# Kernel optimization log

Measured on AMD Instinct MI355X. Metric: run time of the kernel, lower is better.

Reference implementation:

```python
import jax, jax.numpy as jnp
import numpy as np

B, N, K = 4, 20480, 16
LAMDA = 2.0  # config.lfa_param

def _gather(pc, idx):
    # pc: [B, N, D], idx: [B, N, K] -> [B, N, K, D]
    return jax.vmap(lambda p, i: p[i])(pc, idx)

def _cbr(x, W, g, b, act=True):
    # 1x1 conv (no bias) + BN(eval, affine) + optional ReLU; x: [B, C, N, K]
    y = jnp.einsum('oc,bcnk->bonk', W, x)
    y = y * g[None, :, None, None] + b[None, :, None, None]
    return jnp.maximum(y, 0.0) if act else y

def _fdis(feat, f_nb):
    # feat: [B, C, N], f_nb: [B, C, N, K] -> exp(-mean_c |diff|): [B, 1, N, K]
    return jnp.exp(-jnp.mean(jnp.abs(feat[..., None] - f_nb), axis=1, keepdims=True))

def _pool(f_set, f_dis, g_dis, fcW, mW, mg, mb):
    # Dualdis_Att_Pool: softmax attention over neighbor dim K
    concat = jnp.concatenate([g_dis, f_dis * LAMDA, f_set], axis=1)
    att = jax.nn.softmax(jnp.einsum('oc,bcnk->bonk', fcW, concat), axis=3)
    f_lc = jnp.sum(f_set * att, axis=-1, keepdims=True)
    return _cbr(f_lc, mW, mg, mb)

def _forward(feature, xyz, m1_W, m1_g, m1_b, lm1_W, lm1_g, lm1_b, lm2_W, lm2_g, lm2_b, p1fc_W, p1m_W, p1m_g, p1m_b, p2fc_W, p2m_W, p2m_g, p2m_b, m2_W, m2_g, m2_b, sc_W, sc_g, sc_b, m3_W, m3_g, m3_b, m4_W, m4_g, m4_b, neigh_idx):
    f_pc = _cbr(feature, m1_W, m1_g, m1_b)               # [B,16,N,1]
    # --- local polar representation ---
    nb = _gather(xyz, neigh_idx)                         # [B,N,K,3]
    xyz_t = xyz[:, :, None, :]
    rel = xyz_t - nb
    r_alpha = jnp.arctan2(rel[..., 1], rel[..., 0])[..., None]
    r_beta = jnp.arctan2(rel[..., 2], jnp.sqrt(rel[..., 0]**2 + rel[..., 1]**2))[..., None]
    r_dis = jnp.sqrt(jnp.sum(rel * rel, axis=-1, keepdims=True))
    rel_info = jnp.concatenate([r_dis, jnp.broadcast_to(xyz_t, nb.shape), nb], axis=-1)
    g_dis = jnp.exp(-r_dis)                              # [B,N,K,1]
    local_vol = jnp.max(r_dis[..., 0], axis=-1) ** 3     # [B,N]
    dirv = xyz - jnp.mean(nb, axis=2)                    # [B,N,3]
    d_alpha = jnp.arctan2(dirv[..., 1], dirv[..., 0])[:, :, None, None]
    d_beta = jnp.arctan2(dirv[..., 2], jnp.sqrt(dirv[..., 0]**2 + dirv[..., 1]**2))[:, :, None, None]
    angle = jnp.concatenate([r_alpha - d_alpha, r_beta - d_beta], axis=-1)
    local_rep = jnp.concatenate([angle, rel_info], axis=-1)  # [B,N,K,9]
    g_vol = jnp.sqrt(jnp.sum(xyz * xyz, axis=-1)) ** 3
    lg_ratio = (local_vol / g_vol)[..., None]            # [B,N,1]
    g_dis = jnp.transpose(g_dis, (0, 3, 1, 2))           # [B,1,N,K]
    lrep = _cbr(jnp.transpose(local_rep, (0, 3, 1, 2)), lm1_W, lm1_g, lm1_b)  # [B,16,N,K]
    # --- dual-distance attentive pooling 1 ---
    feat0 = f_pc[..., 0]
    f_nb = jnp.transpose(_gather(jnp.transpose(feat0, (0, 2, 1)), neigh_idx), (0, 3, 1, 2))
    f_cat = jnp.concatenate([f_nb, lrep], axis=1)        # [B,32,N,K]
    f_lc = _pool(f_cat, _fdis(feat0, f_nb), g_dis, p1fc_W, p1m_W, p1m_g, p1m_b)  # [B,16,N,1]
    # --- dual-distance attentive pooling 2 ---
    lrep2 = _cbr(lrep, lm2_W, lm2_g, lm2_b)
    feat1 = f_lc[..., 0]
    f_nb2 = jnp.transpose(_gather(jnp.transpose(feat1, (0, 2, 1)), neigh_idx), (0, 3, 1, 2))
    f_cat2 = jnp.concatenate([f_nb2, lrep2], axis=1)     # [B,32,N,K]
    f_lc2 = _pool(f_cat2, _fdis(feat1, f_nb2), g_dis, p2fc_W, p2m_W, p2m_g, p2m_b)  # [B,32,N,1]
    # --- residual head ---
    out_lc = _cbr(f_lc2, m2_W, m2_g, m2_b, act=False)
    sc = _cbr(feature, sc_W, sc_g, sc_b, act=False)
    f_gc_in = jnp.transpose(jnp.concatenate([xyz, lg_ratio], axis=-1), (0, 2, 1))[..., None]
    f_gc = _cbr(f_gc_in, m3_W, m3_g, m3_b, act=False)
    return _cbr(jnp.concatenate([out_lc + sc, f_gc], axis=1), m4_W, m4_g, m4_b)  # [B,64,N,1]

def setup_inputs():
    key = jax.random.key(0)
    ks = iter(jax.random.split(key, 48))
    def rn(shape, s=1.0):
        return jax.random.normal(next(ks), shape, jnp.float32) * s
    inp = {"feature": rn((B, 16, N, 1)), "xyz": rn((B, N, 3))}
    def wgb(name, co, ci):
        inp[name + "_W"] = rn((co, ci), 0.1)
        inp[name + "_g"] = jax.random.uniform(next(ks), (co,), jnp.float32, 0.5, 1.5)
        inp[name + "_b"] = jnp.zeros((co,), jnp.float32)
    wgb("m1", 16, 16); wgb("lm1", 16, 9); wgb("lm2", 16, 16)
    inp["p1fc_W"] = rn((32, 34), 0.1); wgb("p1m", 16, 32)
    inp["p2fc_W"] = rn((32, 34), 0.1); wgb("p2m", 32, 32)
    wgb("m2", 64, 32); wgb("sc", 64, 16); wgb("m3", 64, 4); wgb("m4", 64, 128)
    inp["neigh_idx"] = jax.random.randint(next(ks), (B, N, K), 0, N)
    return inp

def reference(feature, xyz, m1_W, m1_g, m1_b, lm1_W, lm1_g, lm1_b, lm2_W, lm2_g, lm2_b, p1fc_W, p1m_W, p1m_g, p1m_b, p2fc_W, p2m_W, p2m_g, p2m_b, m2_W, m2_g, m2_b, sc_W, sc_g, sc_b, m3_W, m3_g, m3_b, m4_W, m4_g, m4_b, neigh_idx):
    return _forward(feature, xyz, m1_W, m1_g, m1_b, lm1_W, lm1_g, lm1_b, lm2_W, lm2_g, lm2_b, p1fc_W, p1m_W, p1m_g, p1m_b, p2fc_W, p2m_W, p2m_g, p2m_b, m2_W, m2_g, m2_b, sc_W, sc_g, sc_b, m3_W, m3_g, m3_b, m4_W, m4_g, m4_b, neigh_idx)
```

## Files before the change

### kernel.cpp

```cpp
#include <hip/hip_runtime.h>

#define NN 20480
#define NPTS 81920
#define MS 36
#define RSH 40
#define PTSH 640
#define MIDOFF 2560
#define LOG2E 1.4426950408889634f

#define MIDO 0
#define ACTO 2304
#define HO   4608
#define LGRO 13056
#define SMTOT 13120

#define P1MWT 0
#define P2MWT 512
#define M2WT  1536
#define SCWT  3584
#define M3WT  4608
#define M4WT  4864
#define BFB   13056
#define WTOT  15104

typedef _Float16 half8 __attribute__((ext_vector_type(8)));
typedef float f32x4 __attribute__((ext_vector_type(4)));

__device__ __forceinline__ float redsum16(float v){
    v += __shfl_xor(v, 1); v += __shfl_xor(v, 2);
    v += __shfl_xor(v, 4); v += __shfl_xor(v, 8);
    return v;
}
__device__ __forceinline__ float redmax16(float v){
    v = fmaxf(v, __shfl_xor(v, 1)); v = fmaxf(v, __shfl_xor(v, 2));
    v = fmaxf(v, __shfl_xor(v, 4)); v = fmaxf(v, __shfl_xor(v, 8));
    return v;
}
__device__ __forceinline__ void wsync(){
    __builtin_amdgcn_wave_barrier();
    __threadfence_block();
    __builtin_amdgcn_wave_barrier();
}
__device__ __forceinline__ float frcp(float x){ return __builtin_amdgcn_rcpf(x); }

__device__ __forceinline__ unsigned int ph(float lo, float hi){
    union { _Float16 h[2]; unsigned int u; } cv;
    cv.h[0] = (_Float16)lo; cv.h[1] = (_Float16)hi;
    return cv.u;
}
__device__ __forceinline__ float2 unph(unsigned int u){
    union { unsigned int u; _Float16 h[2]; } cv; cv.u = u;
    return make_float2((float)cv.h[0], (float)cv.h[1]);
}
__device__ __forceinline__ float h2f(short s){
    union { short s; _Float16 h; } cv; cv.s = s;
    return (float)cv.h;
}

__device__ __forceinline__ float fatan2(float y, float x){
    float ax = fabsf(x), ay = fabsf(y);
    float mx = fmaxf(ax, ay), mn = fminf(ax, ay);
    float z = mn * frcp(mx);
    z = (mx == 0.f) ? 0.f : z;
    float z2 = z * z;
    float a = fmaf(0.05265332f, z2, -0.11643287f);
    a = fmaf(a, z2, 0.19354346f);
    a = fmaf(a, z2, -0.33262347f);
    a = fmaf(a, z2, 0.99997726f);
    a = a * z;
    a = (ay > ax) ? (1.5707963268f - a) : a;
    a = (x < 0.f) ? (3.1415926536f - a) : a;
    return (y < 0.f) ? -a : a;
}

__device__ __forceinline__ int swiz(int bid){
    int x = bid & 7, s = bid >> 3;
    return ((x >> 1) * 2560) + ((x & 1) * 1280) + s;
}
__device__ __forceinline__ int swizC(int bid){
    int x = bid & 7, s = bid >> 3;
    return x * 160 + s;
}

__global__ void k_fill4(float4* out, float val, int n4){
    int i = blockIdx.x * blockDim.x + threadIdx.x;
    int stride = gridDim.x * blockDim.x;
    float4 v = make_float4(val, val, val, val);
    for (; i < n4; i += stride) out[i] = v;
}

__global__ void k_prep(
    const float* __restrict__ p1fc, const float* __restrict__ p2fc,
    const float* __restrict__ p1mW, const float* __restrict__ p2mW,
    const float* __restrict__ m2W,  const float* __restrict__ scW,
    const float* __restrict__ m3W,  const float* __restrict__ m4W,
    float* __restrict__ wb)
{
    int bid = blockIdx.x;
    if (bid == 0){
        for (int e = threadIdx.x; e < 512; e += 256)
            wb[P1MWT + e] = p1mW[e];
    } else if (bid == 1){
        for (int e = threadIdx.x; e < 1024; e += 256){
            int c = e >> 5, r = e & 31;
            int k = r >> 1, h = r & 1;
            wb[P2MWT + e] = p2mW[(k + 16*h)*32 + c];
        }
    } else if (bid == 2){
        for (int e = threadIdx.x; e < 2048; e += 256){
            int c = e >> 6, r = e & 63;
            int k = r >> 2, j = r & 3;
            wb[M2WT + e] = m2W[(k + 16*j)*32 + c];
        }
    } else if (bid == 3){
        for (int e = threadIdx.x; e < 1024; e += 256){
            int c = e >> 6, r = e & 63;
            int k = r >> 2, j = r & 3;
            wb[SCWT + e] = scW[(k + 16*j)*16 + c];
        }
    } else if (bid == 4){
        for (int e = threadIdx.x; e < 256; e += 256){
            int c = e >> 6, r = e & 63;
            int k = r >> 2, j = r & 3;
            wb[M3WT + e] = m3W[(k + 16*j)*4 + c];
        }
    } else if (bid == 5){
        for (int e = threadIdx.x; e < 8192; e += 256){
            int c = e >> 6, r = e & 63;
            int k = r >> 2, j = r & 3;
            wb[M4WT + e] = m4W[(k + 16*j)*128 + c];
        }
    } else if (bid == 6 || bid == 7){
        const float* src = (bid == 6) ? p1fc : p2fc;
        short* dst = (short*)(wb + BFB) + (bid - 6) * 2048;
        for (int e = threadIdx.x; e < 2048; e += 256){
            int j = e & 7, l = (e >> 3) & 63, tq = (e >> 9) & 3;
            int q = tq & 1, t = tq >> 1;
            int kk = ((l >> 4) << 3) + j;
            int c = q*32 + kk;
            int o = (l & 15) + 16*t;
            float v = (c < 34) ? src[o*34 + c] * LOG2E : 0.f;
            union { _Float16 h; short s; } cv; cv.h = (_Float16)v;
            dst[e] = cv.s;
        }
    }
}

__global__ __launch_bounds__(256) void k_feat0(
    const float* __restrict__ featp,
    const float* __restrict__ m1W,
    const float* __restrict__ m1g,
    const float* __restrict__ m1b,
    float* __restrict__ feat0)
{
    int p = blockIdx.x * 256 + threadIdx.x;
    if (p >= NPTS) return;
    int b = p / NN;
    int n = p - b * NN;
    float x[16];
    #pragma unroll
    for (int c = 0; c < 16; c++) x[c] = featp[(b*16 + c)*NN + n];
    float* dst = feat0 + (size_t)p * 16;
    for (int o = 0; o < 16; o++){
        float acc = 0.f;
        #pragma unroll
        for (int c = 0; c < 16; c++) acc = fmaf(m1W[o*16 + c], x[c], acc);
        dst[o] = fmaxf(fmaf(m1g[o], acc, m1b[o]), 0.f);
    }
}

__device__ __forceinline__ float poolT(f32x4 a, const short* base, int c, int g){
    const short* xc = base + c;
    float x0 = h2f(xc[(g*4 + 0)*RSH]), x1 = h2f(xc[(g*4 + 1)*RSH]);
    float x2 = h2f(xc[(g*4 + 2)*RSH]), x3 = h2f(xc[(g*4 + 3)*RSH]);
    float m = fmaxf(fmaxf(a[0], a[1]), fmaxf(a[2], a[3]));
    m = fmaxf(m, __shfl_xor(m, 16)); m = fmaxf(m, __shfl_xor(m, 32));
    float e0 = exp2f(a[0] - m), e1 = exp2f(a[1] - m);
    float e2 = exp2f(a[2] - m), e3 = exp2f(a[3] - m);
    float s = (e0 + e1) + (e2 + e3);
    float num = fmaf(e3, x3, fmaf(e2, x2, fmaf(e1, x1, e0*x0)));
    s   += __shfl_xor(s, 16);   s   += __shfl_xor(s, 32);
    num += __shfl_xor(num, 16); num += __shfl_xor(num, 32);
    return num * frcp(s);
}

__device__ __forceinline__ void phaseB_mfma(
    const short* xs, const short* bfS, float* smMid, int tid)
{
    const half8* bf = (const half8*)bfS;
    const int l = tid & 63, wv = tid >> 6;
    const int o = l & 15, g = l >> 4;
    half8 B00 = bf[l], B01 = bf[64 + l], B10 = bf[128 + l], B11 = bf[192 + l];
    #pragma unroll 2
    for (int pp = 0; pp < 4; pp++){
        const int pt = wv*4 + pp;
        const short* base = xs + pt*PTSH;
        const short* rowp = base + (l & 15)*RSH;
        half8 A0 = *(const half8*)(rowp + g*8);
        unsigned int d = *(const unsigned int*)(rowp + 32);
        union { unsigned int u[4]; half8 v; } a1u;
        a1u.u[0] = (g == 0) ? d : 0u;
        a1u.u[1] = 0u; a1u.u[2] = 0u; a1u.u[3] = 0u;
        half8 A1 = a1u.v;
        f32x4 z = {0.f, 0.f, 0.f, 0.f};
        f32x4 a0 = __builtin_amdgcn_mfma_f32_16x16x32_f16(A0, B00, z, 0, 0, 0);
        a0       = __builtin_amdgcn_mfma_f32_16x16x32_f16(A1, B01, a0, 0, 0, 0);
        f32x4 a1 = __builtin_amdgcn_mfma_f32_16x16x32_f16(A0, B10, z, 0, 0, 0);
        a1       = __builtin_amdgcn_mfma_f32_16x16x32_f16(A1, B11, a1, 0, 0, 0);
        float mid0 = poolT(a0, base, 2 + o,      g);
        float mid1 = poolT(a1, base, 2 + o + 16, g);
        if (g == 0){
            smMid[pt*MS + o]      = mid0;
            smMid[pt*MS + o + 16] = mid1;
        }
    }
}

__global__ __launch_bounds__(128, 2) void k_stage1(
    const float* __restrict__ xyzp,
    const int* __restrict__ nidx,
    const float* __restrict__ feat0,
    const float* __restrict__ lm1W,
    const float* __restrict__ lm1g,
    const float* __restrict__ lm1b,
    const float* __restrict__ wb,
    const float* __restrict__ p1mg,
    const float* __restrict__ p1mb,
    float* __restrict__ feat1)
{
    __shared__ float sm[2848];
    short* xs = (short*)sm;
    const int k  = threadIdx.x & 15;
    const int pt = threadIdx.x >> 4;
    const int p  = (swiz(blockIdx.x) << 3) + pt;
    const int b  = p / NN;

    {
        const int ii = nidx[(p << 4) + k];
        const int q  = b * NN + ii;
        const float4* an = (const float4*)(feat0 + (size_t)q * 16);
        const float4* as = (const float4*)(feat0 + (size_t)p * 16);
        const float sx = xyzp[p*3 + 0];
        const float sy = xyzp[p*3 + 1];
        const float sz = xyzp[p*3 + 2];
        const float nx = xyzp[q*3 + 0];
        const float ny = xyzp[q*3 + 1];
        const float nz = xyzp[q*3 + 2];

        float4 A0 = an[0], A1 = an[1], A2 = an[2], A3 = an[3];
        float sd = 0.f;
        {
            float4 S0 = as[0], S1 = as[1], S2 = as[2], S3 = as[3];
            sd += fabsf(S0.x-A0.x) + fabsf(S0.y-A0.y) + fabsf(S0.z-A0.z) + fabsf(S0.w-A0.w);
            sd += fabsf(S1.x-A1.x) + fabsf(S1.y-A1.y) + fabsf(S1.z-A1.z) + fabsf(S1.w-A1.w);
            sd += fabsf(S2.x-A2.x) + fabsf(S2.y-A2.y) + fabsf(S2.z-A2.z) + fabsf(S2.w-A2.w);
            sd += fabsf(S3.x-A3.x) + fabsf(S3.y-A3.y) + fabsf(S3.z-A3.z) + fabsf(S3.w-A3.w);
        }
        float fdis2 = 2.f * __expf(-sd * 0.0625f);

        float rx = sx - nx, ry = sy - ny, rz = sz - nz;
        float r2 = rx*rx + ry*ry;
        float rdis = sqrtf(r2 + rz*rz);
        float ralpha = fatan2(ry, rx);
        float rbeta  = fatan2(rz, sqrtf(r2));
        float gdis = __expf(-rdis);

        float mx = redsum16(nx) * 0.0625f;
        float my = redsum16(ny) * 0.0625f;
        float mz = redsum16(nz) * 0.0625f;
        float dx = sx - mx, dy = sy - my, dz = sz - mz;
        float dalpha = fatan2(dy, dx);
        float dbeta  = fatan2(dz, sqrtf(dx*dx + dy*dy));

        float rep[9] = { ralpha - dalpha, rbeta - dbeta, rdis, sx, sy, sz, nx, ny, nz };
        float lrep[16];
        #pragma unroll
        for (int o = 0; o < 16; o++){
            float acc = 0.f;
            #pragma unroll
            for (int c = 0; c < 9; c++) acc = fmaf(lm1W[o*9 + c], rep[c], acc);
            lrep[o] = fmaxf(fmaf(lm1g[o], acc, lm1b[o]), 0.f);
        }

        uint4* rp = (uint4*)(xs + pt*PTSH + k*RSH);
        uint4 U;
        U.x = ph(gdis, fdis2); U.y = ph(A0.x, A0.y);
        U.z = ph(A0.z, A0.w);  U.w = ph(A1.x, A1.y);
        rp[0] = U;
        U.x = ph(A1.z, A1.w);  U.y = ph(A2.x, A2.y);
        U.z = ph(A2.z, A2.w);  U.w = ph(A3.x, A3.y);
        rp[1] = U;
        U.x = ph(A3.z, A3.w);      U.y = ph(lrep[0], lrep[1]);
        U.z = ph(lrep[2], lrep[3]); U.w = ph(lrep[4], lrep[5]);
        rp[2] = U;
        U.x = ph(lrep[6], lrep[7]);   U.y = ph(lrep[8], lrep[9]);
        U.z = ph(lrep[10], lrep[11]); U.w = ph(lrep[12], lrep[13]);
        rp[3] = U;
        U.x = ph(lrep[14], lrep[15]); U.y = 0u; U.z = 0u; U.w = 0u;
        rp[4] = U;
    }
    wsync();

    phaseB_mfma(xs, (const short*)(wb + BFB), sm + MIDOFF, threadIdx.x);
    wsync();

    {
        float mid[32];
        const float4* mp = (const float4*)(sm + MIDOFF + pt*MS);
        #pragma unroll
        for (int i = 0; i < 8; i++){
            float4 t = mp[i];
            mid[4*i]=t.x; mid[4*i+1]=t.y; mid[4*i+2]=t.z; mid[4*i+3]=t.w;
        }
        const float4* wp = (const float4*)(wb + P1MWT) + (k << 3);
        float acc = 0.f;
        #pragma unroll
        for (int i = 0; i < 8; i++){
            float4 wv = wp[i];
            acc = fmaf(wv.x, mid[4*i],   acc);
            acc = fmaf(wv.y, mid[4*i+1], acc);
            acc = fmaf(wv.z, mid[4*i+2], acc);
            acc = fmaf(wv.w, mid[4*i+3], acc);
        }
        feat1[(size_t)(p << 4) + k] = fmaxf(fmaf(p1mg[k], acc, p1mb[k]), 0.f);
    }
}

__global__ __launch_bounds__(128, 2) void k_s2ab(
    const float* __restrict__ xyzp,
    const int* __restrict__ nidx,
    const float* __restrict__ feat1,
    const float* __restrict__ lm1W,
    const float* __restrict__ lm1g,
    const float* __restrict__ lm1b,
    const float* __restrict__ lm2W,
    const float* __restrict__ lm2g,
    const float* __restrict__ lm2b,
    const float* __restrict__ wb,
    float* __restrict__ outp)
{
    __shared__ float sm[2848];
    short* xs = (short*)sm;
    const int k    = threadIdx.x & 15;
    const int pt   = threadIdx.x >> 4;
    const int pblk = swiz(blockIdx.x);
    const int p    = (pblk << 3) + pt;
    const int b    = p / NN;
    const int n    = p - b * NN;
    float lgrv;

    {
        const int ii = nidx[(p << 4) + k];
        const int q  = b * NN + ii;
        const float4* an = (const float4*)(feat1 + (size_t)q * 16);
        const float4* as = (const float4*)(feat1 + (size_t)p * 16);
        const float sx = xyzp[p*3 + 0];
        const float sy = xyzp[p*3 + 1];
        const float sz = xyzp[p*3 + 2];
        const float nx = xyzp[q*3 + 0];
        const float ny = xyzp[q*3 + 1];
        const float nz = xyzp[q*3 + 2];

        float4 A0 = an[0], A1 = an[1], A2 = an[2], A3 = an[3];
        float sd = 0.f;
        {
            float4 S0 = as[0], S1 = as[1], S2 = as[2], S3 = as[3];
            sd += fabsf(S0.x-A0.x) + fabsf(S0.y-A0.y) + fabsf(S0.z-A0.z) + fabsf(S0.w-A0.w);
            sd += fabsf(S1.x-A1.x) + fabsf(S1.y-A1.y) + fabsf(S1.z-A1.z) + fabsf(S1.w-A1.w);
            sd += fabsf(S2.x-A2.x) + fabsf(S2.y-A2.y) + fabsf(S2.z-A2.z) + fabsf(S2.w-A2.w);
            sd += fabsf(S3.x-A3.x) + fabsf(S3.y-A3.y) + fabsf(S3.z-A3.z) + fabsf(S3.w-A3.w);
        }
        float fdis2 = 2.f * __expf(-sd * 0.0625f);

        float rx = sx - nx, ry = sy - ny, rz = sz - nz;
        float r2 = rx*rx + ry*ry;
        float rdis = sqrtf(r2 + rz*rz);
        float ralpha = fatan2(ry, rx);
        float rbeta  = fatan2(rz, sqrtf(r2));
        float gdis = __expf(-rdis);

        float mx = redsum16(nx) * 0.0625f;
        float my = redsum16(ny) * 0.0625f;
        float mz = redsum16(nz) * 0.0625f;
        float dx = sx - mx, dy = sy - my, dz = sz - mz;
        float dalpha = fatan2(dy, dx);
        float dbeta  = fatan2(dz, sqrtf(dx*dx + dy*dy));

        float mxd = redmax16(rdis);
        float nr  = sqrtf(sx*sx + sy*sy + sz*sz);
        lgrv = (mxd*mxd*mxd) * frcp(nr*nr*nr);

        float rep[9] = { ralpha - dalpha, rbeta - dbeta, rdis, sx, sy, sz, nx, ny, nz };
        float lrep[16];
        #pragma unroll
        for (int o = 0; o < 16; o++){
            float acc = 0.f;
            #pragma unroll
            for (int c = 0; c < 9; c++) acc = fmaf(lm1W[o*9 + c], rep[c], acc);
            lrep[o] = fmaxf(fmaf(lm1g[o], acc, lm1b[o]), 0.f);
        }
        float lrep2[16];
        #pragma unroll
        for (int o = 0; o < 16; o++){
            float acc = 0.f;
            #pragma unroll
            for (int c = 0; c < 16; c++) acc = fmaf(lm2W[o*16 + c], lrep[c], acc);
            lrep2[o] = fmaxf(fmaf(lm2g[o], acc, lm2b[o]), 0.f);
        }

        uint4* rp = (uint4*)(xs + pt*PTSH + k*RSH);
        uint4 U;
        U.x = ph(gdis, fdis2); U.y = ph(A0.x, A0.y);
        U.z = ph(A0.z, A0.w);  U.w = ph(A1.x, A1.y);
        rp[0] = U;
        U.x = ph(A1.z, A1.w);  U.y = ph(A2.x, A2.y);
        U.z = ph(A2.z, A2.w);  U.w = ph(A3.x, A3.y);
        rp[1] = U;
        U.x = ph(A3.z, A3.w);        U.y = ph(lrep2[0], lrep2[1]);
        U.z = ph(lrep2[2], lrep2[3]); U.w = ph(lrep2[4], lrep2[5]);
        rp[2] = U;
        U.x = ph(lrep2[6], lrep2[7]);   U.y = ph(lrep2[8], lrep2[9]);
        U.z = ph(lrep2[10], lrep2[11]); U.w = ph(lrep2[12], lrep2[13]);
        rp[3] = U;
        U.x = ph(lrep2[14], lrep2[15]); U.y = 0u; U.z = 0u; U.w = 0u;
        rp[4] = U;
    }
    wsync();

    phaseB_mfma(xs, (const short*)(wb + BFB) + 2048, sm + MIDOFF, threadIdx.x);
    wsync();

    {
        float m0 = sm[MIDOFF + pt*MS + 2*k];
        float m1 = sm[MIDOFF + pt*MS + 2*k + 1];
        unsigned int u = ph(m0, m1);
        ((unsigned int*)outp)[(size_t)(b*64 + k)*NN + n] = u;
        if (k == 0) outp[(size_t)(b*64 + 16)*NN + n] = lgrv;
    }
}

__global__ __launch_bounds__(256, 2) void k_s2c(
    const float* __restrict__ featp,
    const float* __restrict__ xyzp,
    const float* __restrict__ wb,
    const float* __restrict__ p2mg,
    const float* __restrict__ p2mb,
    const float* __restrict__ m2g,
    const float* __restrict__ m2b,
    const float* __restrict__ scg,
    const float* __restrict__ scb,
    const float* __restrict__ m3g,
    const float* __restrict__ m3b,
    const float* __restrict__ m4g,
    const float* __restrict__ m4b,
    float* __restrict__ outp)
{
    __shared__ float sm[SMTOT];
    const int tid = threadIdx.x;
    const int k   = tid & 15;
    const int g   = (tid >> 4) & 3;
    const int w   = tid >> 6;
    const int pblk = swizC(blockIdx.x);
    const int p0  = pblk << 6;
    const int b   = p0 / NN;
    const int n0  = p0 - b * NN;
    const int ptw = w*16 + g*4;
    const int nT  = n0 + ptw;

    {
        uint4 um = *(const uint4*)((const unsigned int*)outp +
                                   (size_t)(b*64 + k)*NN + nT);
        float2 f;
        f = unph(um.x);
        sm[MIDO + (ptw+0)*36 + 2*k] = f.x; sm[MIDO + (ptw+0)*36 + 2*k+1] = f.y;
        f = unph(um.y);
        sm[MIDO + (ptw+1)*36 + 2*k] = f.x; sm[MIDO + (ptw+1)*36 + 2*k+1] = f.y;
        f = unph(um.z);
        sm[MIDO + (ptw+2)*36 + 2*k] = f.x; sm[MIDO + (ptw+2)*36 + 2*k+1] = f.y;
        f = unph(um.w);
        sm[MIDO + (ptw+3)*36 + 2*k] = f.x; sm[MIDO + (ptw+3)*36 + 2*k+1] = f.y;
        if (k == 0){
            float4 lv = *(const float4*)(outp + (size_t)(b*64 + 16)*NN + nT);
            sm[LGRO + ptw+0] = lv.x; sm[LGRO + ptw+1] = lv.y;
            sm[LGRO + ptw+2] = lv.z; sm[LGRO + ptw+3] = lv.w;
        }
    }
    wsync();

    {
        const float2* wp = (const float2*)(wb + P2MWT);
        float aA[4] = {0.f,0.f,0.f,0.f}, aB[4] = {0.f,0.f,0.f,0.f};
        #pragma unroll 2
        for (int cq = 0; cq < 8; cq++){
            f32x4 mv[4];
            #pragma unroll
            for (int i = 0; i < 4; i++)
                mv[i] = *(const f32x4*)(sm + MIDO + (ptw+i)*36 + cq*4);
            #pragma unroll
            for (int cc = 0; cc < 4; cc++){
                float2 wv = wp[(cq*4+cc)*16 + k];
                #pragma unroll
                for (int i = 0; i < 4; i++){
                    aA[i] = fmaf(wv.x, mv[i][cc], aA[i]);
                    aB[i] = fmaf(wv.y, mv[i][cc], aB[i]);
                }
            }
        }
        float gA = p2mg[k], bA = p2mb[k], gB = p2mg[k+16], bB = p2mb[k+16];
        #pragma unroll
        for (int i = 0; i < 4; i++){
            sm[ACTO + (ptw+i)*36 + k]      = fmaxf(fmaf(gA, aA[i], bA), 0.f);
            sm[ACTO + (ptw+i)*36 + k + 16] = fmaxf(fmaf(gB, aB[i], bB), 0.f);
        }
    }
    wsync();

    {
        const f32x4* w2 = (const f32x4*)(wb + M2WT);
        float hAc[4][4];
        #pragma unroll
        for (int j = 0; j < 4; j++)
            #pragma unroll
            for (int i = 0; i < 4; i++) hAc[j][i] = 0.f;
        #pragma unroll 2
        for (int cq = 0; cq < 8; cq++){
            f32x4 av[4];
            #pragma unroll
            for (int i = 0; i < 4; i++)
                av[i] = *(const f32x4*)(sm + ACTO + (ptw+i)*36 + cq*4);
            #pragma unroll
            for (int cc = 0; cc < 4; cc++){
                f32x4 wv = w2[(cq*4+cc)*16 + k];
                #pragma unroll
                for (int i = 0; i < 4; i++){
                    #pragma unroll
                    for (int j = 0; j < 4; j++)
                        hAc[j][i] = fmaf(wv[j], av[i][cc], hAc[j][i]);
                }
            }
        }
        const f32x4* ws = (const f32x4*)(wb + SCWT);
        float sAc[4][4];
        #pragma unroll
        for (int j = 0; j < 4; j++)
            #pragma unroll
            for (int i = 0; i < 4; i++) sAc[j][i] = 0.f;
        #pragma unroll 2
        for (int c = 0; c < 16; c++){
            f32x4 wv = ws[c*16 + k];
            f32x4 xv = *(const f32x4*)(featp + (size_t)(b*16 + c)*NN + nT);
            #pragma unroll
            for (int i = 0; i < 4; i++){
                #pragma unroll
                for (int j = 0; j < 4; j++)
                    sAc[j][i] = fmaf(wv[j], xv[i], sAc[j][i]);
            }
        }
        const f32x4* w3 = (const f32x4*)(wb + M3WT);
        float mAc[4][4];
        #pragma unroll
        for (int j = 0; j < 4; j++)
            #pragma unroll
            for (int i = 0; i < 4; i++) mAc[j][i] = 0.f;
        #pragma unroll
        for (int c = 0; c < 3; c++){
            f32x4 wv = w3[c*16 + k];
            #pragma unroll
            for (int i = 0; i < 4; i++){
                float vc = xyzp[(size_t)(p0 + ptw + i)*3 + c];
                #pragma unroll
                for (int j = 0; j < 4; j++)
                    mAc[j][i] = fmaf(wv[j], vc, mAc[j][i]);
            }
        }
        {
            f32x4 wv = w3[3*16 + k];
            #pragma unroll
            for (int i = 0; i < 4; i++){
                float vc = sm[LGRO + ptw + i];
                #pragma unroll
                for (int j = 0; j < 4; j++)
                    mAc[j][i] = fmaf(wv[j], vc, mAc[j][i]);
            }
        }
        #pragma unroll
        for (int j = 0; j < 4; j++){
            int oo = k + 16*j;
            float g2 = m2g[oo], b2 = m2b[oo];
            float gs = scg[oo], bs = scb[oo];
            float g3 = m3g[oo], b3 = m3b[oo];
            #pragma unroll
            for (int i = 0; i < 4; i++){
                float hv = fmaf(g2, hAc[j][i], b2) + fmaf(gs, sAc[j][i], bs);
                sm[HO + (ptw+i)*132 + oo]      = hv;
                sm[HO + (ptw+i)*132 + 64 + oo] = fmaf(g3, mAc[j][i], b3);
            }
        }
    }
    wsync();

    float acc[4][4];
    #pragma unroll
    for (int j = 0; j < 4; j++)
        #pragma unroll
        for (int i = 0; i < 4; i++) acc[j][i] = 0.f;
    {
        const f32x4* w4 = (const f32x4*)(wb + M4WT);
        #pragma unroll 4
        for (int cb = 0; cb < 32; cb++){
            f32x4 wj[4];
            #pragma unroll
            for (int cc = 0; cc < 4; cc++)
                wj[cc] = w4[(cb*4+cc)*16 + k];
            f32x4 hv[4];
            #pragma unroll
            for (int i = 0; i < 4; i++)
                hv[i] = *(const f32x4*)(sm + HO + (ptw+i)*132 + cb*4);
            #pragma unroll
            for (int cc = 0; cc < 4; cc++){
                #pragma unroll
                for (int i = 0; i < 4; i++){
                    #pragma unroll
                    for (int j = 0; j < 4; j++)
                        acc[j][i] = fmaf(wj[cc][j], hv[i][cc], acc[j][i]);
                }
            }
        }
    }
    {
        float* stg = sm + HO + w*16*132;
        #pragma unroll
        for (int j = 0; j < 4; j++){
            int oo = k + 16*j;
            float gv = m4g[oo], bv = m4b[oo];
            #pragma unroll
            for (int i = 0; i < 4; i++)
                stg[oo*20 + g*4 + i] = fmaxf(fmaf(gv, acc[j][i], bv), 0.f);
        }
        wsync();
        const int l = tid & 63;
        float* dst = outp + (size_t)(b*64 + l)*NN + n0 + w*16;
        #pragma unroll
        for (int q = 0; q < 4; q++){
            f32x4 v = *(const f32x4*)(stg + l*20 + q*4);
            *(f32x4*)(dst + q*4) = v;
        }
    }
}

extern "C" void kernel_launch(void* const* d_in, const int* in_sizes, int n_in,
                              void* d_out, int out_size, void* d_ws, size_t ws_size,
                              hipStream_t stream) {
    float* outp = (float*)d_out;

    float fillv = 1.0f;
    bool ok = true;
    if (n_in != 32) { fillv = 5.0f; ok = false; }
    else if (in_sizes[0] != 1310720 || in_sizes[1] != 245760 ||
             in_sizes[31] != 1310720) { fillv = 7.0f; ok = false; }
    else if (out_size != 5242880) { fillv = 9.0f; ok = false; }
    else if (ws_size < ((size_t)NPTS * 16 + WTOT) * sizeof(float)) { fillv = 11.0f; ok = false; }

    k_fill4<<<1024, 256, 0, stream>>>((float4*)outp, fillv, out_size/4);
    if (!ok) return;

    const float* featp = (const float*)d_in[0];
    const float* xyzp  = (const float*)d_in[1];
    const int*   nidx  = (const int*)d_in[31];

    float* feat0 = (float*)d_out;
    float* feat1 = (float*)d_ws;
    float* wb    = (float*)d_ws + (size_t)NPTS * 16;

    #define W(i) ((const float*)d_in[2 + (i)])
    k_prep<<<8, 256, 0, stream>>>(W(9), W(13), W(10), W(14), W(17), W(20),
                                  W(23), W(26), wb);
    k_feat0<<<NPTS/256, 256, 0, stream>>>(featp, W(0), W(1), W(2), feat0);
    k_stage1<<<NPTS/8, 128, 0, stream>>>(xyzp, nidx, feat0,
        W(3), W(4), W(5), wb, W(11), W(12), feat1);
    k_s2ab<<<NPTS/8, 128, 0, stream>>>(xyzp, nidx, feat1,
        W(3), W(4), W(5),
        W(6), W(7), W(8),
        wb, outp);
    k_s2c<<<NPTS/64, 256, 0, stream>>>(featp, xyzp, wb,
        W(15), W(16),
        W(18), W(19),
        W(21), W(22),
        W(24), W(25),
        W(27), W(28),
        outp);
    #undef W
}
```

Before: 265.9 us.

## Fold m2/sc/m3 linear layers into m4 weights and stage weights in LDS

Since m2, shortcut and m3 are linear with affine BN and no activation before m4, their weights are pre-multiplied into the m4 weights in k_prep, with a folded constant bias. k_s2c then computes the final 64 outputs directly from the activation, feature and xyz inputs, skipping the 128-wide intermediate and its matmul. Folded weights are copied into LDS per block. The output fill kernel now runs only on the error path, and k_feat0 writes with float4 stores. This changes float rounding order and adds a block-wide sync for the weight staging.

```diff
diff --git a/kernel.cpp b/kernel.cpp
--- a/kernel.cpp
+++ b/kernel.cpp
@@ -8,20 +8,24 @@
 #define MIDOFF 2560
 #define LOG2E 1.4426950408889634f
 
-#define MIDO 0
-#define ACTO 2304
-#define HO   4608
-#define LGRO 13056
-#define SMTOT 13120
-
 #define P1MWT 0
 #define P2MWT 512
-#define M2WT  1536
-#define SCWT  3584
-#define M3WT  4608
-#define M4WT  4864
-#define BFB   13056
-#define WTOT  15104
+#define MAWT  1536
+#define MXWT  3584
+#define MVWT  4608
+#define C0WT  4864
+#define BFB   4928
+#define WTOT  6976
+
+#define WL_P2M 0
+#define WL_MA  1024
+#define WL_MX  3072
+#define WL_MV  4096
+#define WL_C0  4352
+#define WOFF   4416
+#define SLAB   1280
+#define LGRO   (WOFF + 4*SLAB)
+#define SMTOT2 9600
 
 typedef _Float16 half8 __attribute__((ext_vector_type(8)));
 typedef float f32x4 __attribute__((ext_vector_type(4)));
@@ -94,6 +98,9 @@
     const float* __restrict__ p1mW, const float* __restrict__ p2mW,
     const float* __restrict__ m2W,  const float* __restrict__ scW,
     const float* __restrict__ m3W,  const float* __restrict__ m4W,
+    const float* __restrict__ m2g,  const float* __restrict__ m2b,
+    const float* __restrict__ scg,  const float* __restrict__ scb,
+    const float* __restrict__ m3g,  const float* __restrict__ m3b,
     float* __restrict__ wb)
 {
     int bid = blockIdx.x;
@@ -109,26 +116,39 @@
     } else if (bid == 2){
         for (int e = threadIdx.x; e < 2048; e += 256){
             int c = e >> 6, r = e & 63;
-            int k = r >> 2, j = r & 3;
-            wb[M2WT + e] = m2W[(k + 16*j)*32 + c];
+            int o = (r >> 2) + 16*(r & 3);
+            float acc = 0.f;
+            for (int h = 0; h < 64; h++)
+                acc = fmaf(m4W[o*128 + h] * m2g[h], m2W[h*32 + c], acc);
+            wb[MAWT + e] = acc;
         }
     } else if (bid == 3){
         for (int e = threadIdx.x; e < 1024; e += 256){
             int c = e >> 6, r = e & 63;
-            int k = r >> 2, j = r & 3;
-            wb[SCWT + e] = scW[(k + 16*j)*16 + c];
+            int o = (r >> 2) + 16*(r & 3);
+            float acc = 0.f;
+            for (int h = 0; h < 64; h++)
+                acc = fmaf(m4W[o*128 + h] * scg[h], scW[h*16 + c], acc);
+            wb[MXWT + e] = acc;
         }
     } else if (bid == 4){
-        for (int e = threadIdx.x; e < 256; e += 256){
+        int e = threadIdx.x;
+        if (e < 256){
             int c = e >> 6, r = e & 63;
-            int k = r >> 2, j = r & 3;
-            wb[M3WT + e] = m3W[(k + 16*j)*4 + c];
-        }
-    } else if (bid == 5){
-        for (int e = threadIdx.x; e < 8192; e += 256){
-            int c = e >> 6, r = e & 63;
-            int k = r >> 2, j = r & 3;
-            wb[M4WT + e] = m4W[(k + 16*j)*128 + c];
+            int o = (r >> 2) + 16*(r & 3);
+            float acc = 0.f;
+            for (int h = 0; h < 64; h++)
+                acc = fmaf(m4W[o*128 + 64 + h] * m3g[h], m3W[h*4 + c], acc);
+            wb[MVWT + e] = acc;
+        }
+        if (e < 64){
+            int o = (e >> 2) + 16*(e & 3);
+            float acc = 0.f;
+            for (int h = 0; h < 64; h++){
+                acc = fmaf(m4W[o*128 + h], m2b[h] + scb[h], acc);
+                acc = fmaf(m4W[o*128 + 64 + h], m3b[h], acc);
+            }
+            wb[C0WT + e] = acc;
         }
     } else if (bid == 6 || bid == 7){
         const float* src = (bid == 6) ? p1fc : p2fc;
@@ -160,13 +180,17 @@
     float x[16];
     #pragma unroll
     for (int c = 0; c < 16; c++) x[c] = featp[(b*16 + c)*NN + n];
-    float* dst = feat0 + (size_t)p * 16;
-    for (int o = 0; o < 16; o++){
+    float o[16];
+    for (int oo = 0; oo < 16; oo++){
         float acc = 0.f;
         #pragma unroll
-        for (int c = 0; c < 16; c++) acc = fmaf(m1W[o*16 + c], x[c], acc);
-        dst[o] = fmaxf(fmaf(m1g[o], acc, m1b[o]), 0.f);
-    }
+        for (int c = 0; c < 16; c++) acc = fmaf(m1W[oo*16 + c], x[c], acc);
+        o[oo] = fmaxf(fmaf(m1g[oo], acc, m1b[oo]), 0.f);
+    }
+    float4* dst = (float4*)(feat0 + (size_t)p * 16);
+    #pragma unroll
+    for (int i = 0; i < 4; i++)
+        dst[i] = make_float4(o[4*i], o[4*i+1], o[4*i+2], o[4*i+3]);
 }
 
 __device__ __forceinline__ float poolT(f32x4 a, const short* base, int c, int g){
@@ -445,17 +469,11 @@
     const float* __restrict__ wb,
     const float* __restrict__ p2mg,
     const float* __restrict__ p2mb,
-    const float* __restrict__ m2g,
-    const float* __restrict__ m2b,
-    const float* __restrict__ scg,
-    const float* __restrict__ scb,
-    const float* __restrict__ m3g,
-    const float* __restrict__ m3b,
     const float* __restrict__ m4g,
     const float* __restrict__ m4b,
     float* __restrict__ outp)
 {
-    __shared__ float sm[SMTOT];
+    __shared__ float sm[SMTOT2];
     const int tid = threadIdx.x;
     const int k   = tid & 15;
     const int g   = (tid >> 4) & 3;
@@ -464,38 +482,40 @@
     const int p0  = pblk << 6;
     const int b   = p0 / NN;
     const int n0  = p0 - b * NN;
-    const int ptw = w*16 + g*4;
-    const int nT  = n0 + ptw;
-
+    const int ptg = g*4;
+    const int nT  = n0 + w*16 + ptg;
+    float* slab = sm + WOFF + w*SLAB;
+
+    for (int e = tid; e < 4416; e += 256) sm[e] = wb[512 + e];
     {
         uint4 um = *(const uint4*)((const unsigned int*)outp +
                                    (size_t)(b*64 + k)*NN + nT);
         float2 f;
         f = unph(um.x);
-        sm[MIDO + (ptw+0)*36 + 2*k] = f.x; sm[MIDO + (ptw+0)*36 + 2*k+1] = f.y;
+        slab[(ptg+0)*36 + 2*k] = f.x; slab[(ptg+0)*36 + 2*k+1] = f.y;
         f = unph(um.y);
-        sm[MIDO + (ptw+1)*36 + 2*k] = f.x; sm[MIDO + (ptw+1)*36 + 2*k+1] = f.y;
+        slab[(ptg+1)*36 + 2*k] = f.x; slab[(ptg+1)*36 + 2*k+1] = f.y;
         f = unph(um.z);
-        sm[MIDO + (ptw+2)*36 + 2*k] = f.x; sm[MIDO + (ptw+2)*36 + 2*k+1] = f.y;
+        slab[(ptg+2)*36 + 2*k] = f.x; slab[(ptg+2)*36 + 2*k+1] = f.y;
         f = unph(um.w);
-        sm[MIDO + (ptw+3)*36 + 2*k] = f.x; sm[MIDO + (ptw+3)*36 + 2*k+1] = f.y;
+        slab[(ptg+3)*36 + 2*k] = f.x; slab[(ptg+3)*36 + 2*k+1] = f.y;
         if (k == 0){
             float4 lv = *(const float4*)(outp + (size_t)(b*64 + 16)*NN + nT);
-            sm[LGRO + ptw+0] = lv.x; sm[LGRO + ptw+1] = lv.y;
-            sm[LGRO + ptw+2] = lv.z; sm[LGRO + ptw+3] = lv.w;
-        }
-    }
-    wsync();
-
-    {
-        const float2* wp = (const float2*)(wb + P2MWT);
+            sm[LGRO + w*16 + ptg + 0] = lv.x; sm[LGRO + w*16 + ptg + 1] = lv.y;
+            sm[LGRO + w*16 + ptg + 2] = lv.z; sm[LGRO + w*16 + ptg + 3] = lv.w;
+        }
+    }
+    __syncthreads();
+
+    {
+        const float2* wp = (const float2*)(sm + WL_P2M);
         float aA[4] = {0.f,0.f,0.f,0.f}, aB[4] = {0.f,0.f,0.f,0.f};
         #pragma unroll 2
         for (int cq = 0; cq < 8; cq++){
             f32x4 mv[4];
             #pragma unroll
             for (int i = 0; i < 4; i++)
-                mv[i] = *(const f32x4*)(sm + MIDO + (ptw+i)*36 + cq*4);
+                mv[i] = *(const f32x4*)(slab + (ptg+i)*36 + cq*4);
             #pragma unroll
             for (int cc = 0; cc < 4; cc++){
                 float2 wv = wp[(cq*4+cc)*16 + k];
@@ -509,133 +529,84 @@
         float gA = p2mg[k], bA = p2mb[k], gB = p2mg[k+16], bB = p2mb[k+16];
         #pragma unroll
         for (int i = 0; i < 4; i++){
-            sm[ACTO + (ptw+i)*36 + k]      = fmaxf(fmaf(gA, aA[i], bA), 0.f);
-            sm[ACTO + (ptw+i)*36 + k + 16] = fmaxf(fmaf(gB, aB[i], bB), 0.f);
+            slab[576 + (ptg+i)*36 + k]      = fmaxf(fmaf(gA, aA[i], bA), 0.f);
+            slab[576 + (ptg+i)*36 + k + 16] = fmaxf(fmaf(gB, aB[i], bB), 0.f);
         }
     }
     wsync();
 
-    {
-        const f32x4* w2 = (const f32x4*)(wb + M2WT);
-        float hAc[4][4];
+    float o4[4][4];
+    {
+        f32x4 c0v = *(const f32x4*)(sm + WL_C0 + 4*k);
         #pragma unroll
         for (int j = 0; j < 4; j++)
             #pragma unroll
-            for (int i = 0; i < 4; i++) hAc[j][i] = 0.f;
+            for (int i = 0; i < 4; i++) o4[j][i] = c0v[j];
+
+        const f32x4* wa = (const f32x4*)(sm + WL_MA);
         #pragma unroll 2
         for (int cq = 0; cq < 8; cq++){
             f32x4 av[4];
             #pragma unroll
             for (int i = 0; i < 4; i++)
-                av[i] = *(const f32x4*)(sm + ACTO + (ptw+i)*36 + cq*4);
+                av[i] = *(const f32x4*)(slab + 576 + (ptg+i)*36 + cq*4);
             #pragma unroll
             for (int cc = 0; cc < 4; cc++){
-                f32x4 wv = w2[(cq*4+cc)*16 + k];
+                f32x4 wv = wa[(cq*4+cc)*16 + k];
                 #pragma unroll
                 for (int i = 0; i < 4; i++){
                     #pragma unroll
                     for (int j = 0; j < 4; j++)
-                        hAc[j][i] = fmaf(wv[j], av[i][cc], hAc[j][i]);
+                        o4[j][i] = fmaf(wv[j], av[i][cc], o4[j][i]);
                 }
             }
         }
-        const f32x4* ws = (const f32x4*)(wb + SCWT);
-        float sAc[4][4];
-        #pragma unroll
-        for (int j = 0; j < 4; j++)
-            #pragma unroll
-            for (int i = 0; i < 4; i++) sAc[j][i] = 0.f;
-        #pragma unroll 2
+        const f32x4* wx = (const f32x4*)(sm + WL_MX);
+        #pragma unroll 4
         for (int c = 0; c < 16; c++){
-            f32x4 wv = ws[c*16 + k];
+            f32x4 wv = wx[c*16 + k];
             f32x4 xv = *(const f32x4*)(featp + (size_t)(b*16 + c)*NN + nT);
             #pragma unroll
             for (int i = 0; i < 4; i++){
                 #pragma unroll
                 for (int j = 0; j < 4; j++)
-                    sAc[j][i] = fmaf(wv[j], xv[i], sAc[j][i]);
+                    o4[j][i] = fmaf(wv[j], xv[i], o4[j][i]);
             }
         }
-        const f32x4* w3 = (const f32x4*)(wb + M3WT);
-        float mAc[4][4];
-        #pragma unroll
-        for (int j = 0; j < 4; j++)
-            #pragma unroll
-            for (int i = 0; i < 4; i++) mAc[j][i] = 0.f;
+        const f32x4* wvv = (const f32x4*)(sm + WL_MV);
         #pragma unroll
         for (int c = 0; c < 3; c++){
-            f32x4 wv = w3[c*16 + k];
+            f32x4 wv = wvv[c*16 + k];
             #pragma unroll
             for (int i = 0; i < 4; i++){
-                float vc = xyzp[(size_t)(p0 + ptw + i)*3 + c];
+                float vc = xyzp[(size_t)(p0 + w*16 + ptg + i)*3 + c];
                 #pragma unroll
                 for (int j = 0; j < 4; j++)
-                    mAc[j][i] = fmaf(wv[j], vc, mAc[j][i]);
+                    o4[j][i] = fmaf(wv[j], vc, o4[j][i]);
             }
         }
         {
-            f32x4 wv = w3[3*16 + k];
+            f32x4 wv = wvv[3*16 + k];
             #pragma unroll
             for (int i = 0; i < 4; i++){
-                float vc = sm[LGRO + ptw + i];
+                float vc = sm[LGRO + w*16 + ptg + i];
                 #pragma unroll
                 for (int j = 0; j < 4; j++)
-                    mAc[j][i] = fmaf(wv[j], vc, mAc[j][i]);
+                    o4[j][i] = fmaf(wv[j], vc, o4[j][i]);
             }
         }
-        #pragma unroll
-        for (int j = 0; j < 4; j++){
-            int oo = k + 16*j;
-            float g2 = m2g[oo], b2 = m2b[oo];
-            float gs = scg[oo], bs = scb[oo];
-            float g3 = m3g[oo], b3 = m3b[oo];
-            #pragma unroll
-            for (int i = 0; i < 4; i++){
-                float hv = fmaf(g2, hAc[j][i], b2) + fmaf(gs, sAc[j][i], bs);
-                sm[HO + (ptw+i)*132 + oo]      = hv;
-                sm[HO + (ptw+i)*132 + 64 + oo] = fmaf(g3, mAc[j][i], b3);
-            }
-        }
     }
     wsync();
 
-    float acc[4][4];
-    #pragma unroll
-    for (int j = 0; j < 4; j++)
-        #pragma unroll
-        for (int i = 0; i < 4; i++) acc[j][i] = 0.f;
-    {
-        const f32x4* w4 = (const f32x4*)(wb + M4WT);
-        #pragma unroll 4
-        for (int cb = 0; cb < 32; cb++){
-            f32x4 wj[4];
-            #pragma unroll
-            for (int cc = 0; cc < 4; cc++)
-                wj[cc] = w4[(cb*4+cc)*16 + k];
-            f32x4 hv[4];
-            #pragma unroll
-            for (int i = 0; i < 4; i++)
-                hv[i] = *(const f32x4*)(sm + HO + (ptw+i)*132 + cb*4);
-            #pragma unroll
-            for (int cc = 0; cc < 4; cc++){
-                #pragma unroll
-                for (int i = 0; i < 4; i++){
-                    #pragma unroll
-                    for (int j = 0; j < 4; j++)
-                        acc[j][i] = fmaf(wj[cc][j], hv[i][cc], acc[j][i]);
-                }
-            }
-        }
-    }
-    {
-        float* stg = sm + HO + w*16*132;
+    {
+        float* stg = slab;
         #pragma unroll
         for (int j = 0; j < 4; j++){
             int oo = k + 16*j;
             float gv = m4g[oo], bv = m4b[oo];
             #pragma unroll
             for (int i = 0; i < 4; i++)
-                stg[oo*20 + g*4 + i] = fmaxf(fmaf(gv, acc[j][i], bv), 0.f);
+                stg[oo*20 + ptg + i] = fmaxf(fmaf(gv, o4[j][i], bv), 0.f);
         }
         wsync();
         const int l = tid & 63;
@@ -661,8 +632,10 @@
     else if (out_size != 5242880) { fillv = 9.0f; ok = false; }
     else if (ws_size < ((size_t)NPTS * 16 + WTOT) * sizeof(float)) { fillv = 11.0f; ok = false; }
 
-    k_fill4<<<1024, 256, 0, stream>>>((float4*)outp, fillv, out_size/4);
-    if (!ok) return;
+    if (!ok){
+        k_fill4<<<1024, 256, 0, stream>>>((float4*)outp, fillv, out_size/4);
+        return;
+    }
 
     const float* featp = (const float*)d_in[0];
     const float* xyzp  = (const float*)d_in[1];
@@ -674,7 +647,9 @@
 
     #define W(i) ((const float*)d_in[2 + (i)])
     k_prep<<<8, 256, 0, stream>>>(W(9), W(13), W(10), W(14), W(17), W(20),
-                                  W(23), W(26), wb);
+                                  W(23), W(26),
+                                  W(18), W(19), W(21), W(22), W(24), W(25),
+                                  wb);
     k_feat0<<<NPTS/256, 256, 0, stream>>>(featp, W(0), W(1), W(2), feat0);
     k_stage1<<<NPTS/8, 128, 0, stream>>>(xyzp, nidx, feat0,
         W(3), W(4), W(5), wb, W(11), W(12), feat1);
@@ -684,9 +659,6 @@
         wb, outp);
     k_s2c<<<NPTS/64, 256, 0, stream>>>(featp, xyzp, wb,
         W(15), W(16),
-        W(18), W(19),
-        W(21), W(22),
-        W(24), W(25),
         W(27), W(28),
         outp);
     #undef W
```

Result: faster. 253.7 us (-4.6%).
